# Performance work log

Measured on AMD Instinct MI355X. Metric: run time of the kernel, lower is better.

The kernel has to match this reference:

```python
import jax, jax.numpy as jnp
import numpy as np

L_LAYERS = 2
SEQ = 2048
K_EIG = 24
D = 128
D_TGT = 64
K_U = 3
K_Y = 2
B = 8


def hankel_eigh(n, k):
    # Z[i,j] = 2 / ((i+j)^3 - (i+j)), 1-indexed; top-k eigenpairs
    s = np.arange(1, n + 1, dtype=np.float64)
    ij = s[:, None] + s[None, :]
    z = 2.0 / (ij ** 3 - ij)
    vals, vecs = np.linalg.eigh(z)
    return (jnp.asarray(vals[-k:], jnp.float32), jnp.asarray(vecs[:, -k:], jnp.float32))


def setup_inputs() -> dict:
    key = jax.random.key(0)
    ks = jax.random.split(key, 8)
    sd = 1.0 / np.sqrt(D)
    inp = {
        "x": jax.random.normal(ks[0], (B, SEQ, D), jnp.float32),
        "emb_w": jax.random.normal(ks[1], (D, D), jnp.float32) * sd,
        "emb_b": jnp.zeros((D,), jnp.float32),
        "ln_g": jnp.ones((L_LAYERS, D), jnp.float32),
        "ln_b": jnp.zeros((L_LAYERS, D), jnp.float32),
        "m_phi": jax.random.normal(ks[2], (L_LAYERS, K_EIG * D, D), jnp.float32) * sd,
        "m_u": jax.random.normal(ks[3], (L_LAYERS, D, D, K_U), jnp.float32) * sd,
        "m_y": jax.random.normal(ks[4], (L_LAYERS, D, K_Y, D), jnp.float32) * 0.01,
        "w1": jax.random.normal(ks[5], (L_LAYERS, D, 2 * D), jnp.float32) * sd,
        "b1": jnp.zeros((L_LAYERS, 2 * D), jnp.float32),
        "proj_w": jax.random.normal(ks[6], (D, D_TGT), jnp.float32) * sd,
        "proj_b": jnp.zeros((D_TGT,), jnp.float32),
    }
    ev, evec = hankel_eigh(SEQ, K_EIG)
    inp["eig_vals"] = ev
    inp["eig_vecs"] = evec
    return inp


def compute_x_tilde(x, eig_vals, eig_vecs):
    # x: [B, L, D]; causal (truncated full) convolution of each eigvec filter
    # with each input channel via FFT. Result [B, L, K, D] -> [B, L, K*D].
    n = 2 * SEQ
    V = jnp.fft.rfft(eig_vecs, n=n, axis=0)              # [nf, K]
    U = jnp.fft.rfft(x, n=n, axis=1)                     # [B, nf, D]
    conv = jnp.fft.irfft(V[None, :, :, None] * U[:, :, None, :], n=n, axis=1)[:, :SEQ]
    conv = conv * (eig_vals ** 0.25)[None, None, :, None]
    return conv.reshape(x.shape[0], SEQ, K_EIG * x.shape[-1]).astype(x.dtype)


def compute_ar_x_preds(m_u, x):
    # o[t] = sum_{i<K_U} m_u[:, :, i] @ x[t-i]  (zero for t-i < 0)
    res = jnp.einsum('bli,oi->blo', x, m_u[:, :, 0])
    for i in range(1, K_U):
        xi = jnp.pad(x, ((0, 0), (i, 0), (0, 0)))[:, :SEQ]
        res = res + jnp.einsum('bli,oi->blo', xi, m_u[:, :, i])
    return res


def compute_y_t(m_y, deltas):
    # y[t] = sum_{j<K_Y} m_y[:, j, :] @ y[t-1-j] + deltas[t]
    d = deltas.shape[-1]
    def step(carry, x):  # carry [B, K_Y, d] holds y[t-1], y[t-2], ...
        out = jnp.einsum('okd,bkd->bo', m_y, carry) + x
        carry = jnp.concatenate([out[:, None, :], carry[:, :-1]], axis=1)
        return carry, out
    init = jnp.zeros((deltas.shape[0], K_Y, d), deltas.dtype)
    _, ys = jax.lax.scan(step, init, jnp.swapaxes(deltas, 0, 1))
    return jnp.swapaxes(ys, 0, 1)


def layer_norm(x, g, b):
    mu = x.mean(-1, keepdims=True)
    var = ((x - mu) ** 2).mean(-1, keepdims=True)
    return (x - mu) / jnp.sqrt(var + 1e-5) * g + b


def reference(x, emb_w, emb_b, ln_g, ln_b, m_phi, m_u, m_y, w1, b1, proj_w, proj_b, eig_vals, eig_vecs):
    h = x @ emb_w + emb_b
    for i in range(L_LAYERS):
        z = h
        h = layer_norm(h, ln_g[i], ln_b[i])
        x_tilde = compute_x_tilde(h, eig_vals, eig_vecs)       # [B, L, K*D]
        delta = x_tilde @ m_phi[i] + compute_ar_x_preds(m_u[i], h)
        y = compute_y_t(m_y[i], delta)
        y = jax.nn.gelu(y, approximate=False)
        y = y @ w1[i] + b1[i]
        a, g = jnp.split(y, 2, axis=-1)
        h = a * jax.nn.sigmoid(g) + z                          # GLU + residual (dropout=0)
    return h @ proj_w + proj_b
```

## Files before the change

### kernel.cpp

```cpp
#include <hip/hip_runtime.h>

typedef unsigned short u16;
typedef unsigned int u32;
typedef __bf16 bf16x8 __attribute__((ext_vector_type(8)));
typedef float f32x4 __attribute__((ext_vector_type(4)));
typedef float f32x2 __attribute__((ext_vector_type(2)));
typedef u16 u16x4 __attribute__((ext_vector_type(4)));
typedef u16 u16x8 __attribute__((ext_vector_type(8)));

#define DEV static __device__ __forceinline__

static constexpr int ROWS = 8 * 2048;
static constexpr int TAPS = 24;
static constexpr int PADR = 64;
static constexpr int DROWS = 2048 + PADR;

DEV u16 f2bf(float x) {
  u32 u = __float_as_uint(x);
  u += 0x7fffu + ((u >> 16) & 1u);
  return (u16)(u >> 16);
}

DEV void gld_lds16(const u16* g, u16* l) {
  __builtin_amdgcn_global_load_lds(
      (const __attribute__((address_space(1))) u32*)g,
      (__attribute__((address_space(3))) u32*)l, 16, 0, 0);
}


__global__ void prep_toeplitz(const float* __restrict__ evec,
                              const float* __restrict__ evals,
                              u16* __restrict__ T) {
  int k = blockIdx.x / 33, ti = blockIdx.x % 33;
  float sc = powf(evals[k], 0.25f);
  u16* out = T + (size_t)blockIdx.x * 4096;
  for (int e = threadIdx.x; e < 4096; e += 256) {
    int i = e >> 6, j = e & 63;
    int tau = (ti - 1) * 64 + i - j;
    float v = (tau >= 0 && tau < 2048) ? evec[tau * 24 + k] * sc : 0.f;
    out[e] = f2bf(v);
  }
}

__global__ void transpose_w(const float* __restrict__ src, u16* __restrict__ dst,
                            int K, int N) {
  int idx = blockIdx.x * 256 + threadIdx.x;
  if (idx >= K * N) return;
  int n = idx / K, k = idx % K;
  dst[idx] = f2bf(src[(size_t)k * N + n]);
}

__global__ void prep_mphiT(const float* __restrict__ mphi,
                           const float* __restrict__ mu,
                           u16* __restrict__ dst) {
  int idx = blockIdx.x * 256 + threadIdx.x;
  if (idx >= 128 * 3456) return;
  int o = idx / 3456, c = idx % 3456;
  float v;
  if (c < 3072) {
    v = mphi[(size_t)c * 128 + o];
  } else {
    int cc = c - 3072;
    int j = cc >> 7, i = cc & 127;
    v = mu[((size_t)o * 128 + i) * 3 + j];
  }
  dst[idx] = f2bf(v);
}

__global__ void f32_to_bf16_k(const float* __restrict__ src, u16* __restrict__ dst,
                              int n4) {
  int i = blockIdx.x * 256 + threadIdx.x;
  if (i >= n4) return;
  f32x4 v = *(const f32x4*)(src + (size_t)i * 4);
  u16x4 o;
  o[0] = f2bf(v[0]); o[1] = f2bf(v[1]); o[2] = f2bf(v[2]); o[3] = f2bf(v[3]);
  *(u16x4*)(dst + (size_t)i * 4) = o;
}

__global__ __launch_bounds__(128) void hprep_kernel(const float* __restrict__ my,
                                                    u16* __restrict__ Hp) {
  const int l = blockIdx.x >> 7, j = blockIdx.x & 127;
  const int o = threadIdx.x;
  const float* M = my + (size_t)l * 32768;
  u32 mp1[64], mp2[64];
  {
    const float* r1 = M + (size_t)o * 256;
    const float* r2 = r1 + 128;
#pragma unroll
    for (int q = 0; q < 64; ++q) {
      mp1[q] = (u32)f2bf(r1[2 * q]) | ((u32)f2bf(r1[2 * q + 1]) << 16);
      mp2[q] = (u32)f2bf(r2[2 * q]) | ((u32)f2bf(r2[2 * q + 1]) << 16);
    }
  }
  __shared__ float vb[3][128];
  u16* HpL = Hp + ((size_t)l * 128 + o) * (TAPS * 128) + j;
  float v0 = (o == j) ? 1.f : 0.f;
  vb[0][o] = v0;
  vb[2][o] = 0.f;
  HpL[0] = f2bf(v0);
  __syncthreads();
  for (int tau = 1; tau < TAPS; ++tau) {
    const int a = (tau + 2) % 3;
    const int b = (tau + 1) % 3;
    const int c = tau % 3;
    const float* v1 = vb[a];
    const float* v2 = vb[b];
    float acc = 0.f;
#pragma unroll
    for (int q = 0; q < 64; ++q) {
      u32 w1 = mp1[q], w2 = mp2[q];
      float m1lo = __uint_as_float(w1 << 16);
      float m1hi = __uint_as_float(w1 & 0xffff0000u);
      float m2lo = __uint_as_float(w2 << 16);
      float m2hi = __uint_as_float(w2 & 0xffff0000u);
      acc += m1lo * v1[2 * q] + m1hi * v1[2 * q + 1];
      acc += m2lo * v2[2 * q] + m2hi * v2[2 * q + 1];
    }
    vb[c][o] = acc;
    HpL[tau * 128] = f2bf(acc);
    __syncthreads();
  }
}

__global__ void zero_pad(u16* __restrict__ dpad) {
  int i = blockIdx.x * 256 + threadIdx.x;
  int b = i >> 10, off = i & 1023;
  *(u16x8*)(dpad + (size_t)b * DROWS * 128 + off * 8) = (u16x8){0, 0, 0, 0, 0, 0, 0, 0};
}


__global__ __launch_bounds__(256) void ln_tr_kernel(
    const float* __restrict__ h, const float* __restrict__ gam,
    const float* __restrict__ bet, u16* __restrict__ hlnbf,
    u16* __restrict__ hlnT) {
  __shared__ u16 tile[64][136];
  const int b = blockIdx.x >> 5, st = blockIdx.x & 31;
  const int wrow = threadIdx.x >> 6;
  const int lane = threadIdx.x & 63;
  f32x2 g2 = *(const f32x2*)(gam + lane * 2);
  f32x2 b2 = *(const f32x2*)(bet + lane * 2);
#pragma unroll 4
  for (int it = 0; it < 16; ++it) {
    int lr = it * 4 + wrow;
    size_t row = (size_t)b * 2048 + st * 64 + lr;
    f32x2 v = *(const f32x2*)(h + row * 128 + lane * 2);
    float s = v[0] + v[1];
#pragma unroll
    for (int o = 32; o; o >>= 1) s += __shfl_xor(s, o);
    float mu = s * (1.f / 128.f);
    float dx = v[0] - mu, dy = v[1] - mu;
    float q = dx * dx + dy * dy;
#pragma unroll
    for (int o = 32; o; o >>= 1) q += __shfl_xor(q, o);
    float rstd = rsqrtf(q * (1.f / 128.f) + 1e-5f);
    float o0 = dx * rstd * g2[0] + b2[0];
    float o1 = dy * rstd * g2[1] + b2[1];
    u32 pk = (u32)f2bf(o0) | ((u32)f2bf(o1) << 16);
    *(u32*)(hlnbf + row * 128 + lane * 2) = pk;
    *(u32*)&tile[lr][lane * 2] = pk;
  }
  __syncthreads();
  const int d = threadIdx.x >> 1;
  const int half = threadIdx.x & 1;
#pragma unroll
  for (int i = 0; i < 4; ++i) {
    int sg = half * 4 + i;
    u16x8 w;
#pragma unroll
    for (int j = 0; j < 8; ++j) w[j] = tile[sg * 8 + j][d];
    *(u16x8*)(hlnT + ((size_t)b * 128 + d) * 2048 + st * 64 + sg * 8) = w;
  }
}

__global__ void shift_kernel(const u16* __restrict__ hln, u16* __restrict__ xtc) {
  int row = blockIdx.x;
  int t = row & 2047;
  int d = threadIdx.x;
#pragma unroll
  for (int j = 0; j < 3; ++j) {
    u16 v = (t >= j) ? hln[(size_t)(row - j) * 128 + d] : (u16)0;
    xtc[(size_t)row * 3456 + 3072 + j * 128 + d] = v;
  }
}


template <int BM, int BN, int WROWS, int WCOLS>
__global__ __launch_bounds__(256) void gemm_bt(
    const u16* __restrict__ A, int lda, const u16* __restrict__ BT, int ldbt,
    float* __restrict__ C, int ldc, const float* __restrict__ bias, int kBlocks,
    u16* __restrict__ Cbf) {
  constexpr int WTM = BM / WROWS;
  constexpr int WTN = BN / WCOLS;
  constexpr int FM = WTM / 16;
  constexpr int FN = WTN / 16;
  static_assert(FM >= 1 && FN >= 1, "tile too small");
  __shared__ u16 As[BM * 64];
  __shared__ u16 Bs[BN * 64];
  const int tid = threadIdx.x;
  const int wid = tid >> 6, lane = tid & 63;
  const int bm = blockIdx.x, bn = blockIdx.y;
  const int wr = wid / WCOLS, wc = wid % WCOLS;
  const int r = lane & 15, hi = lane >> 4;

  f32x4 acc[FM][FN];
#pragma unroll
  for (int i = 0; i < FM; ++i)
#pragma unroll
    for (int j = 0; j < FN; ++j) acc[i][j] = (f32x4){0.f, 0.f, 0.f, 0.f};

  for (int kb = 0; kb < kBlocks; ++kb) {
    if (kb) __syncthreads();
#pragma unroll
    for (int it = 0; it < BM / 32; ++it) {
      int ci = it * 256 + tid;
      int sc = (ci & 7) ^ ((ci >> 3) & 7);
      gld_lds16(A + (size_t)(bm * BM + (ci >> 3)) * lda + kb * 64 + sc * 8,
                &As[(it * 256 + wid * 64) * 8]);
    }
#pragma unroll
    for (int it = 0; it < BN / 32; ++it) {
      int ci = it * 256 + tid;
      int sc = (ci & 7) ^ ((ci >> 3) & 7);
      gld_lds16(BT + (size_t)(bn * BN + (ci >> 3)) * ldbt + kb * 64 + sc * 8,
                &Bs[(it * 256 + wid * 64) * 8]);
    }
    __syncthreads();
#pragma unroll
    for (int ks = 0; ks < 2; ++ks) {
      const int sk = ((ks * 4 + hi) ^ (r & 7)) << 3;
      bf16x8 af[FM], bfv[FN];
#pragma unroll
      for (int fm = 0; fm < FM; ++fm)
        af[fm] = *(const bf16x8*)&As[(wr * WTM + fm * 16 + r) * 64 + sk];
#pragma unroll
      for (int fn = 0; fn < FN; ++fn)
        bfv[fn] = *(const bf16x8*)&Bs[(wc * WTN + fn * 16 + r) * 64 + sk];
#pragma unroll
      for (int fm = 0; fm < FM; ++fm)
#pragma unroll
        for (int fn = 0; fn < FN; ++fn)
          acc[fm][fn] = __builtin_amdgcn_mfma_f32_16x16x32_bf16(
              af[fm], bfv[fn], acc[fm][fn], 0, 0, 0);
    }
  }
#pragma unroll
  for (int fm = 0; fm < FM; ++fm) {
#pragma unroll
    for (int fn = 0; fn < FN; ++fn) {
      const int col = bn * BN + wc * WTN + fn * 16 + r;
      const float bv = bias ? bias[col] : 0.f;
#pragma unroll
      for (int q = 0; q < 4; ++q) {
        const int row = bm * BM + wr * WTM + fm * 16 + hi * 4 + q;
        float v = acc[fm][fn][q] + bv;
        if (Cbf) {
          int bb = row >> 11, t = row & 2047;
          Cbf[((size_t)(bb * DROWS + PADR + t)) * 128 + col] = f2bf(v);
        } else {
          C[(size_t)row * ldc + col] = v;
        }
      }
    }
  }
}

__global__ __launch_bounds__(256) void gemm_conv(
    const u16* __restrict__ T, const u16* __restrict__ hlnT,
    u16* __restrict__ xtc) {
  __shared__ u16 As[128 * 64];
  __shared__ u16 Bs[128 * 64];
  const int tid = threadIdx.x;
  const int wid = tid >> 6, lane = tid & 63;
  const int tt = blockIdx.x / 192;
  const int rem = blockIdx.x % 192;
  const int kc = rem >> 3, b = rem & 7;
  const int t0 = (15 - tt) << 7;
  const int r = lane & 15, hi = lane >> 4;
  const int wr = wid >> 1, wc = wid & 1;

  f32x4 acc[4][4];
#pragma unroll
  for (int i = 0; i < 4; ++i)
#pragma unroll
    for (int j = 0; j < 4; ++j) acc[i][j] = (f32x4){0.f, 0.f, 0.f, 0.f};

  const u16* Tk = T + (size_t)kc * 33 * 4096;
  const u16* Bb = hlnT + (size_t)b * 128 * 2048;
  const int nsb = (t0 >> 6) + 2;

  for (int sb = 0; sb < nsb; ++sb) {
    const int dlt = (t0 >> 6) - sb;
    if (sb) __syncthreads();
#pragma unroll
    for (int it = 0; it < 4; ++it) {
      int ci = it * 256 + tid;
      int ti = (ci < 512) ? (dlt + 1) : (dlt + 2);
      int lc = ci & 511;
      int sc = (lc & 7) ^ ((lc >> 3) & 7);
      gld_lds16(Tk + (size_t)ti * 4096 + (lc >> 3) * 64 + sc * 8,
                &As[(it * 256 + wid * 64) * 8]);
    }
#pragma unroll
    for (int it = 0; it < 4; ++it) {
      int ci = it * 256 + tid;
      int sc = (ci & 7) ^ ((ci >> 3) & 7);
      gld_lds16(Bb + (size_t)(ci >> 3) * 2048 + sb * 64 + sc * 8,
                &Bs[(it * 256 + wid * 64) * 8]);
    }
    __syncthreads();
#pragma unroll
    for (int ks = 0; ks < 2; ++ks) {
      const int sk = ((ks * 4 + hi) ^ (r & 7)) << 3;
      bf16x8 af[4], bfv[4];
#pragma unroll
      for (int fm = 0; fm < 4; ++fm)
        af[fm] = *(const bf16x8*)&As[(wr * 64 + fm * 16 + r) * 64 + sk];
#pragma unroll
      for (int fn = 0; fn < 4; ++fn)
        bfv[fn] = *(const bf16x8*)&Bs[(wc * 64 + fn * 16 + r) * 64 + sk];
#pragma unroll
      for (int fm = 0; fm < 4; ++fm)
#pragma unroll
        for (int fn = 0; fn < 4; ++fn)
          acc[fm][fn] = __builtin_amdgcn_mfma_f32_16x16x32_bf16(
              af[fm], bfv[fn], acc[fm][fn], 0, 0, 0);
    }
  }
#pragma unroll
  for (int fm = 0; fm < 4; ++fm) {
#pragma unroll
    for (int fn = 0; fn < 4; ++fn) {
      const int col = wc * 64 + fn * 16 + r;
#pragma unroll
      for (int q = 0; q < 4; ++q) {
        const int row = t0 + wr * 64 + fm * 16 + hi * 4 + q;
        xtc[((size_t)(b * 2048 + row)) * 3456 + kc * 128 + col] = f2bf(acc[fm][fn][q]);
      }
    }
  }
}

__global__ __launch_bounds__(256) void gemm_yconv(
    const u16* __restrict__ dpad, const u16* __restrict__ Hp,
    u16* __restrict__ ybf) {
  __shared__ u16 As[64 * 64];
  __shared__ u16 Bs[64 * 64];
  const int tid = threadIdx.x;
  const int wid = tid >> 6, lane = tid & 63;
  const int bm = blockIdx.x, bn = blockIdx.y;
  const int b = bm >> 5, t0 = (bm & 31) << 6;
  const int r = lane & 15, hi = lane >> 4;

  f32x4 acc[4];
#pragma unroll
  for (int j = 0; j < 4; ++j) acc[j] = (f32x4){0.f, 0.f, 0.f, 0.f};

  const u16* Ab = dpad + (size_t)b * DROWS * 128;
  for (int kb = 0; kb < TAPS * 2; ++kb) {
    const int tap = kb >> 1, i0 = (kb & 1) << 6;
    const u16* Ap = Ab + (size_t)(PADR + t0 - tap) * 128 + i0;
    if (kb) __syncthreads();
#pragma unroll
    for (int it = 0; it < 2; ++it) {
      int ci = it * 256 + tid;
      int sc = (ci & 7) ^ ((ci >> 3) & 7);
      gld_lds16(Ap + (size_t)(ci >> 3) * 128 + sc * 8,
                &As[(it * 256 + wid * 64) * 8]);
    }
#pragma unroll
    for (int it = 0; it < 2; ++it) {
      int ci = it * 256 + tid;
      int sc = (ci & 7) ^ ((ci >> 3) & 7);
      gld_lds16(Hp + (size_t)(bn * 64 + (ci >> 3)) * (TAPS * 128) + kb * 64 + sc * 8,
                &Bs[(it * 256 + wid * 64) * 8]);
    }
    __syncthreads();
#pragma unroll
    for (int ks = 0; ks < 2; ++ks) {
      const int sk = ((ks * 4 + hi) ^ (r & 7)) << 3;
      bf16x8 af = *(const bf16x8*)&As[(wid * 16 + r) * 64 + sk];
      bf16x8 bfv[4];
#pragma unroll
      for (int fn = 0; fn < 4; ++fn)
        bfv[fn] = *(const bf16x8*)&Bs[(fn * 16 + r) * 64 + sk];
#pragma unroll
      for (int fn = 0; fn < 4; ++fn)
        acc[fn] = __builtin_amdgcn_mfma_f32_16x16x32_bf16(af, bfv[fn], acc[fn], 0, 0, 0);
    }
  }
#pragma unroll
  for (int fn = 0; fn < 4; ++fn) {
    const int col = bn * 64 + fn * 16 + r;
#pragma unroll
    for (int q = 0; q < 4; ++q) {
      const int row = t0 + wid * 16 + hi * 4 + q;
      float v = acc[fn][q];
      float gl = 0.5f * v * (1.f + erff(v * 0.70710678118654752f));
      ybf[((size_t)(b * 2048 + row)) * 128 + col] = f2bf(gl);
    }
  }
}

__global__ __launch_bounds__(256) void gemm_w1glu(
    const u16* __restrict__ ybf, const u16* __restrict__ w1T,
    const float* __restrict__ b1, float* __restrict__ h,
    u16* __restrict__ hbf) {
  __shared__ u16 As[32 * 64];
  __shared__ u16 Bs[256 * 64];
  __shared__ float sg[32][128];
  const int tid = threadIdx.x;
  const int wid = tid >> 6, lane = tid & 63;
  const int bm = blockIdx.x;
  const int wr = wid >> 1, wc = wid & 1;
  const int r = lane & 15, hi = lane >> 4;

  f32x4 acc[8];
#pragma unroll
  for (int j = 0; j < 8; ++j) acc[j] = (f32x4){0.f, 0.f, 0.f, 0.f};

  for (int kb = 0; kb < 2; ++kb) {
    if (kb) __syncthreads();
    {
      int ci = tid;
      int sc = (ci & 7) ^ ((ci >> 3) & 7);
      gld_lds16(ybf + (size_t)(bm * 32 + (ci >> 3)) * 128 + kb * 64 + sc * 8,
                &As[(wid * 64) * 8]);
    }
#pragma unroll
    for (int it = 0; it < 8; ++it) {
      int ci = it * 256 + tid;
      int sc = (ci & 7) ^ ((ci >> 3) & 7);
      gld_lds16(w1T + (size_t)(ci >> 3) * 128 + kb * 64 + sc * 8,
                &Bs[(it * 256 + wid * 64) * 8]);
    }
    __syncthreads();
#pragma unroll
    for (int ks = 0; ks < 2; ++ks) {
      const int sk = ((ks * 4 + hi) ^ (r & 7)) << 3;
      bf16x8 af = *(const bf16x8*)&As[(wr * 16 + r) * 64 + sk];
      bf16x8 bfv[8];
#pragma unroll
      for (int fn = 0; fn < 8; ++fn)
        bfv[fn] = *(const bf16x8*)&Bs[(wc * 128 + fn * 16 + r) * 64 + sk];
#pragma unroll
      for (int fn = 0; fn < 8; ++fn)
        acc[fn] = __builtin_amdgcn_mfma_f32_16x16x32_bf16(af, bfv[fn], acc[fn], 0, 0, 0);
    }
  }
  __syncthreads();
  if (wc == 1) {
#pragma unroll
    for (int fn = 0; fn < 8; ++fn) {
      const int colg = fn * 16 + r;
      const float bv = b1[128 + colg];
#pragma unroll
      for (int q = 0; q < 4; ++q) {
        const int rl = wr * 16 + hi * 4 + q;
        float v = acc[fn][q] + bv;
        sg[rl][colg] = 1.f / (1.f + expf(-v));
      }
    }
  }
  __syncthreads();
  if (wc == 0) {
#pragma unroll
    for (int fn = 0; fn < 8; ++fn) {
      const int col = fn * 16 + r;
      const float bv = b1[col];
#pragma unroll
      for (int q = 0; q < 4; ++q) {
        const int rl = wr * 16 + hi * 4 + q;
        const size_t row = (size_t)bm * 32 + rl;
        float a = acc[fn][q] + bv;
        float hn = a * sg[rl][col] + h[row * 128 + col];
        h[row * 128 + col] = hn;
        hbf[row * 128 + col] = f2bf(hn);
      }
    }
  }
}


extern "C" void kernel_launch(void* const* d_in, const int* in_sizes, int n_in,
                              void* d_out, int out_size, void* d_ws, size_t ws_size,
                              hipStream_t stream) {
  (void)in_sizes; (void)n_in; (void)out_size; (void)ws_size;
  const float* x = (const float*)d_in[0];
  const float* emb_w = (const float*)d_in[1];
  const float* emb_b = (const float*)d_in[2];
  const float* ln_g = (const float*)d_in[3];
  const float* ln_b = (const float*)d_in[4];
  const float* m_phi = (const float*)d_in[5];
  const float* m_u = (const float*)d_in[6];
  const float* m_y = (const float*)d_in[7];
  const float* w1 = (const float*)d_in[8];
  const float* b1 = (const float*)d_in[9];
  const float* proj_w = (const float*)d_in[10];
  const float* proj_b = (const float*)d_in[11];
  const float* evals = (const float*)d_in[12];
  const float* evec = (const float*)d_in[13];
  float* out = (float*)d_out;

  char* p = (char*)d_ws;
  auto carve = [&](size_t bytes) {
    char* r = p;
    p += (bytes + 255) & ~(size_t)255;
    return r;
  };
  u16* Tbuf = (u16*)carve((size_t)24 * 33 * 4096 * 2);
  u16* embT = (u16*)carve(128 * 128 * 2);
  u16* w1T = (u16*)carve((size_t)2 * 256 * 128 * 2);
  u16* projT = (u16*)carve(64 * 128 * 2);
  u16* mphiT = (u16*)carve((size_t)2 * 128 * 3456 * 2);
  u16* Hp = (u16*)carve((size_t)2 * 128 * TAPS * 128 * 2);
  u16* xbf = (u16*)carve((size_t)ROWS * 128 * 2);
  float* h = (float*)carve((size_t)ROWS * 128 * 4);
  u16* hbf = (u16*)carve((size_t)ROWS * 128 * 2);
  u16* hlnbf = (u16*)carve((size_t)ROWS * 128 * 2);
  u16* hlnT = (u16*)carve((size_t)ROWS * 128 * 2);
  u16* xtc = (u16*)carve((size_t)ROWS * 3456 * 2);
  u16* dpad = (u16*)carve((size_t)8 * DROWS * 128 * 2);
  u16* ybf = (u16*)carve((size_t)ROWS * 128 * 2);

  prep_toeplitz<<<dim3(24 * 33), dim3(256), 0, stream>>>(evec, evals, Tbuf);
  hprep_kernel<<<dim3(256), dim3(128), 0, stream>>>(m_y, Hp);
  zero_pad<<<dim3(32), dim3(256), 0, stream>>>(dpad);
  transpose_w<<<dim3(64), dim3(256), 0, stream>>>(emb_w, embT, 128, 128);
  transpose_w<<<dim3(128), dim3(256), 0, stream>>>(w1, w1T, 128, 256);
  transpose_w<<<dim3(128), dim3(256), 0, stream>>>(w1 + 128 * 256, w1T + 256 * 128, 128, 256);
  transpose_w<<<dim3(32), dim3(256), 0, stream>>>(proj_w, projT, 128, 64);
  prep_mphiT<<<dim3(1728), dim3(256), 0, stream>>>(m_phi, m_u, mphiT);
  prep_mphiT<<<dim3(1728), dim3(256), 0, stream>>>(
      m_phi + (size_t)3072 * 128, m_u + (size_t)128 * 128 * 3, mphiT + (size_t)128 * 3456);
  f32_to_bf16_k<<<dim3(2048), dim3(256), 0, stream>>>(x, xbf, ROWS * 128 / 4);

  gemm_bt<32, 128, 2, 2><<<dim3(512, 1), dim3(256), 0, stream>>>(
      xbf, 128, embT, 128, h, 128, emb_b, 2, nullptr);

  for (int l = 0; l < 2; ++l) {
    const u16* mT = mphiT + (size_t)l * 128 * 3456;
    ln_tr_kernel<<<dim3(256), dim3(256), 0, stream>>>(
        h, ln_g + l * 128, ln_b + l * 128, hlnbf, hlnT);
    shift_kernel<<<dim3(16384), dim3(128), 0, stream>>>(hlnbf, xtc);
    gemm_conv<<<dim3(3072), dim3(256), 0, stream>>>(Tbuf, hlnT, xtc);
    gemm_bt<32, 128, 2, 2><<<dim3(512, 1), dim3(256), 0, stream>>>(
        xtc, 3456, mT, 3456, nullptr, 0, nullptr, 54, dpad);
    gemm_yconv<<<dim3(256, 2), dim3(256), 0, stream>>>(
        dpad, Hp + (size_t)l * 128 * TAPS * 128, ybf);
    gemm_w1glu<<<dim3(512), dim3(256), 0, stream>>>(
        ybf, w1T + (size_t)l * 256 * 128, b1 + l * 256, h, hbf);
  }

  gemm_bt<32, 64, 2, 2><<<dim3(512, 1), dim3(256), 0, stream>>>(
      hbf, 128, projT, 128, out, 64, proj_b, 2, nullptr);
}
```

Measured before the change: 506.7 us.

## Merge prep kernels, fuse shift into layernorm, double-buffer delta and conv GEMMs

Merges the weight-transpose, conversion and zero-padding prep kernels into one prep_misc launch. The layernorm kernel now writes the shifted autoregressive columns straight into xtc, which removes shift_kernel and the hlnbf buffer. The delta GEMM becomes a dedicated double-buffered kernel that writes bf16 into the padded buffer. gemm_conv reuses the Toeplitz tile from the previous step through a ping-pong A buffer, halving its A loads, and gemm_yconv processes a full 128-wide tap per iteration, halving the sync count. These changes add LDS use and index complexity in exchange for fewer launches and less memory traffic.

```diff
diff --git a/kernel.cpp b/kernel.cpp
--- a/kernel.cpp
+++ b/kernel.cpp
@@ -40,41 +40,6 @@
     float v = (tau >= 0 && tau < 2048) ? evec[tau * 24 + k] * sc : 0.f;
     out[e] = f2bf(v);
   }
-}
-
-__global__ void transpose_w(const float* __restrict__ src, u16* __restrict__ dst,
-                            int K, int N) {
-  int idx = blockIdx.x * 256 + threadIdx.x;
-  if (idx >= K * N) return;
-  int n = idx / K, k = idx % K;
-  dst[idx] = f2bf(src[(size_t)k * N + n]);
-}
-
-__global__ void prep_mphiT(const float* __restrict__ mphi,
-                           const float* __restrict__ mu,
-                           u16* __restrict__ dst) {
-  int idx = blockIdx.x * 256 + threadIdx.x;
-  if (idx >= 128 * 3456) return;
-  int o = idx / 3456, c = idx % 3456;
-  float v;
-  if (c < 3072) {
-    v = mphi[(size_t)c * 128 + o];
-  } else {
-    int cc = c - 3072;
-    int j = cc >> 7, i = cc & 127;
-    v = mu[((size_t)o * 128 + i) * 3 + j];
-  }
-  dst[idx] = f2bf(v);
-}
-
-__global__ void f32_to_bf16_k(const float* __restrict__ src, u16* __restrict__ dst,
-                              int n4) {
-  int i = blockIdx.x * 256 + threadIdx.x;
-  if (i >= n4) return;
-  f32x4 v = *(const f32x4*)(src + (size_t)i * 4);
-  u16x4 o;
-  o[0] = f2bf(v[0]); o[1] = f2bf(v[1]); o[2] = f2bf(v[2]); o[3] = f2bf(v[3]);
-  *(u16x4*)(dst + (size_t)i * 4) = o;
 }
 
 __global__ __launch_bounds__(128) void hprep_kernel(const float* __restrict__ my,
@@ -122,17 +87,67 @@
   }
 }
 
-__global__ void zero_pad(u16* __restrict__ dpad) {
-  int i = blockIdx.x * 256 + threadIdx.x;
-  int b = i >> 10, off = i & 1023;
-  *(u16x8*)(dpad + (size_t)b * DROWS * 128 + off * 8) = (u16x8){0, 0, 0, 0, 0, 0, 0, 0};
+__global__ __launch_bounds__(256) void prep_misc(
+    const float* __restrict__ emb_w, const float* __restrict__ w1,
+    const float* __restrict__ proj_w, const float* __restrict__ mphi,
+    const float* __restrict__ mu, const float* __restrict__ x,
+    u16* __restrict__ embT, u16* __restrict__ w1T, u16* __restrict__ projT,
+    u16* __restrict__ mphiT, u16* __restrict__ xbf, u16* __restrict__ dpad,
+    u16* __restrict__ xtc) {
+  const int blk = blockIdx.x, tid = threadIdx.x;
+  if (blk < 64) {
+    int idx = blk * 256 + tid;
+    int n = idx >> 7, k = idx & 127;
+    embT[idx] = f2bf(emb_w[k * 128 + n]);
+  } else if (blk < 320) {
+    int l = (blk - 64) >> 7;
+    int idx = ((blk - 64) & 127) * 256 + tid;
+    int n = idx >> 7, k = idx & 127;
+    w1T[l * 32768 + idx] = f2bf(w1[l * 32768 + k * 256 + n]);
+  } else if (blk < 352) {
+    int idx = (blk - 320) * 256 + tid;
+    int n = idx >> 7, k = idx & 127;
+    projT[idx] = f2bf(proj_w[k * 64 + n]);
+  } else if (blk < 3808) {
+    int l = (blk - 352) / 1728;
+    int idx = ((blk - 352) % 1728) * 256 + tid;
+    int o = idx / 3456, c = idx % 3456;
+    float v;
+    if (c < 3072) {
+      v = mphi[(size_t)l * 3072 * 128 + (size_t)c * 128 + o];
+    } else {
+      int cc = c - 3072;
+      int j = cc >> 7, i = cc & 127;
+      v = mu[(size_t)l * 128 * 128 * 3 + ((size_t)o * 128 + i) * 3 + j];
+    }
+    mphiT[(size_t)l * 128 * 3456 + idx] = f2bf(v);
+  } else if (blk < 5856) {
+    int i = (blk - 3808) * 256 + tid;
+    f32x4 v = *(const f32x4*)(x + (size_t)i * 4);
+    u16x4 o;
+    o[0] = f2bf(v[0]); o[1] = f2bf(v[1]); o[2] = f2bf(v[2]); o[3] = f2bf(v[3]);
+    *(u16x4*)(xbf + (size_t)i * 4) = o;
+  } else if (blk < 5888) {
+    int i = (blk - 5856) * 256 + tid;
+    int b = i >> 10, off = i & 1023;
+    *(u16x8*)(dpad + (size_t)b * DROWS * 128 + off * 8) =
+        (u16x8){0, 0, 0, 0, 0, 0, 0, 0};
+  } else {
+    for (int e = tid; e < 3072; e += 256) {
+      int b = e / 384, r = e % 384;
+      size_t addr;
+      if (r < 256) addr = ((size_t)b * 2048 + 0) * 3456 + 3200 + r;
+      else addr = ((size_t)b * 2048 + 1) * 3456 + 3328 + (r - 256);
+      xtc[addr] = 0;
+    }
+  }
 }
 
 
 __global__ __launch_bounds__(256) void ln_tr_kernel(
     const float* __restrict__ h, const float* __restrict__ gam,
-    const float* __restrict__ bet, u16* __restrict__ hlnbf,
-    u16* __restrict__ hlnT) {
+    const float* __restrict__ bet, u16* __restrict__ hlnT,
+    u16* __restrict__ xtc) {
   __shared__ u16 tile[64][136];
   const int b = blockIdx.x >> 5, st = blockIdx.x & 31;
   const int wrow = threadIdx.x >> 6;
@@ -142,7 +157,8 @@
 #pragma unroll 4
   for (int it = 0; it < 16; ++it) {
     int lr = it * 4 + wrow;
-    size_t row = (size_t)b * 2048 + st * 64 + lr;
+    int t = st * 64 + lr;
+    size_t row = (size_t)b * 2048 + t;
     f32x2 v = *(const f32x2*)(h + row * 128 + lane * 2);
     float s = v[0] + v[1];
 #pragma unroll
@@ -156,8 +172,10 @@
     float o0 = dx * rstd * g2[0] + b2[0];
     float o1 = dy * rstd * g2[1] + b2[1];
     u32 pk = (u32)f2bf(o0) | ((u32)f2bf(o1) << 16);
-    *(u32*)(hlnbf + row * 128 + lane * 2) = pk;
     *(u32*)&tile[lr][lane * 2] = pk;
+    *(u32*)&xtc[row * 3456 + 3072 + lane * 2] = pk;
+    if (t + 1 < 2048) *(u32*)&xtc[(row + 1) * 3456 + 3200 + lane * 2] = pk;
+    if (t + 2 < 2048) *(u32*)&xtc[(row + 2) * 3456 + 3328 + lane * 2] = pk;
   }
   __syncthreads();
   const int d = threadIdx.x >> 1;
@@ -172,23 +190,11 @@
   }
 }
 
-__global__ void shift_kernel(const u16* __restrict__ hln, u16* __restrict__ xtc) {
-  int row = blockIdx.x;
-  int t = row & 2047;
-  int d = threadIdx.x;
-#pragma unroll
-  for (int j = 0; j < 3; ++j) {
-    u16 v = (t >= j) ? hln[(size_t)(row - j) * 128 + d] : (u16)0;
-    xtc[(size_t)row * 3456 + 3072 + j * 128 + d] = v;
-  }
-}
-
 
 template <int BM, int BN, int WROWS, int WCOLS>
 __global__ __launch_bounds__(256) void gemm_bt(
     const u16* __restrict__ A, int lda, const u16* __restrict__ BT, int ldbt,
-    float* __restrict__ C, int ldc, const float* __restrict__ bias, int kBlocks,
-    u16* __restrict__ Cbf) {
+    float* __restrict__ C, int ldc, const float* __restrict__ bias, int kBlocks) {
   constexpr int WTM = BM / WROWS;
   constexpr int WTN = BN / WCOLS;
   constexpr int FM = WTM / 16;
@@ -252,14 +258,70 @@
 #pragma unroll
       for (int q = 0; q < 4; ++q) {
         const int row = bm * BM + wr * WTM + fm * 16 + hi * 4 + q;
-        float v = acc[fm][fn][q] + bv;
-        if (Cbf) {
-          int bb = row >> 11, t = row & 2047;
-          Cbf[((size_t)(bb * DROWS + PADR + t)) * 128 + col] = f2bf(v);
-        } else {
-          C[(size_t)row * ldc + col] = v;
-        }
+        C[(size_t)row * ldc + col] = acc[fm][fn][q] + bv;
       }
+    }
+  }
+}
+
+__global__ __launch_bounds__(256) void gemm_delta(
+    const u16* __restrict__ A, const u16* __restrict__ BT,
+    u16* __restrict__ dpad) {
+  __shared__ u16 As[2][32 * 64];
+  __shared__ u16 Bs[2][128 * 64];
+  const int tid = threadIdx.x;
+  const int wid = tid >> 6, lane = tid & 63;
+  const int bm = blockIdx.x;
+  const int wr = wid >> 1, wc = wid & 1;
+  const int r = lane & 15, hi = lane >> 4;
+
+  f32x4 acc[4];
+#pragma unroll
+  for (int j = 0; j < 4; ++j) acc[j] = (f32x4){0.f, 0.f, 0.f, 0.f};
+
+  auto stage = [&](int kb, int p) {
+    {
+      int ci = tid;
+      int sc = (ci & 7) ^ ((ci >> 3) & 7);
+      gld_lds16(A + (size_t)(bm * 32 + (ci >> 3)) * 3456 + kb * 64 + sc * 8,
+                &As[p][(wid * 64) * 8]);
+    }
+#pragma unroll
+    for (int it = 0; it < 4; ++it) {
+      int ci = it * 256 + tid;
+      int sc = (ci & 7) ^ ((ci >> 3) & 7);
+      gld_lds16(BT + (size_t)(ci >> 3) * 3456 + kb * 64 + sc * 8,
+                &Bs[p][(it * 256 + wid * 64) * 8]);
+    }
+  };
+
+  stage(0, 0);
+  __syncthreads();
+  for (int kb = 0; kb < 54; ++kb) {
+    const int p = kb & 1;
+    if (kb < 53) stage(kb + 1, p ^ 1);
+#pragma unroll
+    for (int ks = 0; ks < 2; ++ks) {
+      const int sk = ((ks * 4 + hi) ^ (r & 7)) << 3;
+      bf16x8 af = *(const bf16x8*)&As[p][(wr * 16 + r) * 64 + sk];
+      bf16x8 bfv[4];
+#pragma unroll
+      for (int fn = 0; fn < 4; ++fn)
+        bfv[fn] = *(const bf16x8*)&Bs[p][(wc * 64 + fn * 16 + r) * 64 + sk];
+#pragma unroll
+      for (int fn = 0; fn < 4; ++fn)
+        acc[fn] = __builtin_amdgcn_mfma_f32_16x16x32_bf16(af, bfv[fn], acc[fn], 0, 0, 0);
+    }
+    __syncthreads();
+  }
+#pragma unroll
+  for (int fn = 0; fn < 4; ++fn) {
+    const int col = wc * 64 + fn * 16 + r;
+#pragma unroll
+    for (int q = 0; q < 4; ++q) {
+      const int row = bm * 32 + wr * 16 + hi * 4 + q;
+      int bb = row >> 11, t = row & 2047;
+      dpad[((size_t)(bb * DROWS + PADR + t)) * 128 + col] = f2bf(acc[fn][q]);
     }
   }
 }
@@ -267,7 +329,7 @@
 __global__ __launch_bounds__(256) void gemm_conv(
     const u16* __restrict__ T, const u16* __restrict__ hlnT,
     u16* __restrict__ xtc) {
-  __shared__ u16 As[128 * 64];
+  __shared__ u16 As[2][64 * 64];
   __shared__ u16 Bs[128 * 64];
   const int tid = threadIdx.x;
   const int wid = tid >> 6, lane = tid & 63;
@@ -286,19 +348,28 @@
 
   const u16* Tk = T + (size_t)kc * 33 * 4096;
   const u16* Bb = hlnT + (size_t)b * 128 * 2048;
-  const int nsb = (t0 >> 6) + 2;
+  const int base = t0 >> 6;
+  const int nsb = base + 2;
 
   for (int sb = 0; sb < nsb; ++sb) {
-    const int dlt = (t0 >> 6) - sb;
+    const int dlt = base - sb;
+    const int p = sb & 1;
     if (sb) __syncthreads();
 #pragma unroll
-    for (int it = 0; it < 4; ++it) {
-      int ci = it * 256 + tid;
-      int ti = (ci < 512) ? (dlt + 1) : (dlt + 2);
-      int lc = ci & 511;
-      int sc = (lc & 7) ^ ((lc >> 3) & 7);
-      gld_lds16(Tk + (size_t)ti * 4096 + (lc >> 3) * 64 + sc * 8,
-                &As[(it * 256 + wid * 64) * 8]);
+    for (int it = 0; it < 2; ++it) {
+      int ci = it * 256 + tid;
+      int sc = (ci & 7) ^ ((ci >> 3) & 7);
+      gld_lds16(Tk + (size_t)(dlt + 1) * 4096 + (ci >> 3) * 64 + sc * 8,
+                &As[p][(it * 256 + wid * 64) * 8]);
+    }
+    if (sb == 0) {
+#pragma unroll
+      for (int it = 0; it < 2; ++it) {
+        int ci = it * 256 + tid;
+        int sc = (ci & 7) ^ ((ci >> 3) & 7);
+        gld_lds16(Tk + (size_t)(dlt + 2) * 4096 + (ci >> 3) * 64 + sc * 8,
+                  &As[1][(it * 256 + wid * 64) * 8]);
+      }
     }
 #pragma unroll
     for (int it = 0; it < 4; ++it) {
@@ -308,13 +379,14 @@
                 &Bs[(it * 256 + wid * 64) * 8]);
     }
     __syncthreads();
+    const u16* Aw = As[p ^ wr];
 #pragma unroll
     for (int ks = 0; ks < 2; ++ks) {
       const int sk = ((ks * 4 + hi) ^ (r & 7)) << 3;
       bf16x8 af[4], bfv[4];
 #pragma unroll
       for (int fm = 0; fm < 4; ++fm)
-        af[fm] = *(const bf16x8*)&As[(wr * 64 + fm * 16 + r) * 64 + sk];
+        af[fm] = *(const bf16x8*)&Aw[(fm * 16 + r) * 64 + sk];
 #pragma unroll
       for (int fn = 0; fn < 4; ++fn)
         bfv[fn] = *(const bf16x8*)&Bs[(wc * 64 + fn * 16 + r) * 64 + sk];
@@ -343,8 +415,8 @@
 __global__ __launch_bounds__(256) void gemm_yconv(
     const u16* __restrict__ dpad, const u16* __restrict__ Hp,
     u16* __restrict__ ybf) {
-  __shared__ u16 As[64 * 64];
-  __shared__ u16 Bs[64 * 64];
+  __shared__ u16 As[64 * 128];
+  __shared__ u16 Bs[64 * 128];
   const int tid = threadIdx.x;
   const int wid = tid >> 6, lane = tid & 63;
   const int bm = blockIdx.x, bn = blockIdx.y;
@@ -356,33 +428,34 @@
   for (int j = 0; j < 4; ++j) acc[j] = (f32x4){0.f, 0.f, 0.f, 0.f};
 
   const u16* Ab = dpad + (size_t)b * DROWS * 128;
-  for (int kb = 0; kb < TAPS * 2; ++kb) {
-    const int tap = kb >> 1, i0 = (kb & 1) << 6;
-    const u16* Ap = Ab + (size_t)(PADR + t0 - tap) * 128 + i0;
-    if (kb) __syncthreads();
-#pragma unroll
-    for (int it = 0; it < 2; ++it) {
-      int ci = it * 256 + tid;
-      int sc = (ci & 7) ^ ((ci >> 3) & 7);
-      gld_lds16(Ap + (size_t)(ci >> 3) * 128 + sc * 8,
+  for (int tap = 0; tap < TAPS; ++tap) {
+    const u16* Ap = Ab + (size_t)(PADR + t0 - tap) * 128;
+    if (tap) __syncthreads();
+#pragma unroll
+    for (int it = 0; it < 4; ++it) {
+      int ci = it * 256 + tid;
+      int row = ci >> 4;
+      int sc = (ci & 15) ^ (row & 7);
+      gld_lds16(Ap + (size_t)row * 128 + sc * 8,
                 &As[(it * 256 + wid * 64) * 8]);
     }
 #pragma unroll
-    for (int it = 0; it < 2; ++it) {
-      int ci = it * 256 + tid;
-      int sc = (ci & 7) ^ ((ci >> 3) & 7);
-      gld_lds16(Hp + (size_t)(bn * 64 + (ci >> 3)) * (TAPS * 128) + kb * 64 + sc * 8,
+    for (int it = 0; it < 4; ++it) {
+      int ci = it * 256 + tid;
+      int row = ci >> 4;
+      int sc = (ci & 15) ^ (row & 7);
+      gld_lds16(Hp + (size_t)(bn * 64 + row) * (TAPS * 128) + tap * 128 + sc * 8,
                 &Bs[(it * 256 + wid * 64) * 8]);
     }
     __syncthreads();
 #pragma unroll
-    for (int ks = 0; ks < 2; ++ks) {
+    for (int ks = 0; ks < 4; ++ks) {
       const int sk = ((ks * 4 + hi) ^ (r & 7)) << 3;
-      bf16x8 af = *(const bf16x8*)&As[(wid * 16 + r) * 64 + sk];
+      bf16x8 af = *(const bf16x8*)&As[(wid * 16 + r) * 128 + sk];
       bf16x8 bfv[4];
 #pragma unroll
       for (int fn = 0; fn < 4; ++fn)
-        bfv[fn] = *(const bf16x8*)&Bs[(fn * 16 + r) * 64 + sk];
+        bfv[fn] = *(const bf16x8*)&Bs[(fn * 16 + r) * 128 + sk];
 #pragma unroll
       for (int fn = 0; fn < 4; ++fn)
         acc[fn] = __builtin_amdgcn_mfma_f32_16x16x32_bf16(af, bfv[fn], acc[fn], 0, 0, 0);
@@ -516,7 +589,6 @@
   u16* xbf = (u16*)carve((size_t)ROWS * 128 * 2);
   float* h = (float*)carve((size_t)ROWS * 128 * 4);
   u16* hbf = (u16*)carve((size_t)ROWS * 128 * 2);
-  u16* hlnbf = (u16*)carve((size_t)ROWS * 128 * 2);
   u16* hlnT = (u16*)carve((size_t)ROWS * 128 * 2);
   u16* xtc = (u16*)carve((size_t)ROWS * 3456 * 2);
   u16* dpad = (u16*)carve((size_t)8 * DROWS * 128 * 2);
@@ -524,27 +596,18 @@
 
   prep_toeplitz<<<dim3(24 * 33), dim3(256), 0, stream>>>(evec, evals, Tbuf);
   hprep_kernel<<<dim3(256), dim3(128), 0, stream>>>(m_y, Hp);
-  zero_pad<<<dim3(32), dim3(256), 0, stream>>>(dpad);
-  transpose_w<<<dim3(64), dim3(256), 0, stream>>>(emb_w, embT, 128, 128);
-  transpose_w<<<dim3(128), dim3(256), 0, stream>>>(w1, w1T, 128, 256);
-  transpose_w<<<dim3(128), dim3(256), 0, stream>>>(w1 + 128 * 256, w1T + 256 * 128, 128, 256);
-  transpose_w<<<dim3(32), dim3(256), 0, stream>>>(proj_w, projT, 128, 64);
-  prep_mphiT<<<dim3(1728), dim3(256), 0, stream>>>(m_phi, m_u, mphiT);
-  prep_mphiT<<<dim3(1728), dim3(256), 0, stream>>>(
-      m_phi + (size_t)3072 * 128, m_u + (size_t)128 * 128 * 3, mphiT + (size_t)128 * 3456);
-  f32_to_bf16_k<<<dim3(2048), dim3(256), 0, stream>>>(x, xbf, ROWS * 128 / 4);
+  prep_misc<<<dim3(5889), dim3(256), 0, stream>>>(
+      emb_w, w1, proj_w, m_phi, m_u, x, embT, w1T, projT, mphiT, xbf, dpad, xtc);
 
   gemm_bt<32, 128, 2, 2><<<dim3(512, 1), dim3(256), 0, stream>>>(
-      xbf, 128, embT, 128, h, 128, emb_b, 2, nullptr);
+      xbf, 128, embT, 128, h, 128, emb_b, 2);
 
   for (int l = 0; l < 2; ++l) {
     const u16* mT = mphiT + (size_t)l * 128 * 3456;
     ln_tr_kernel<<<dim3(256), dim3(256), 0, stream>>>(
-        h, ln_g + l * 128, ln_b + l * 128, hlnbf, hlnT);
-    shift_kernel<<<dim3(16384), dim3(128), 0, stream>>>(hlnbf, xtc);
+        h, ln_g + l * 128, ln_b + l * 128, hlnT, xtc);
     gemm_conv<<<dim3(3072), dim3(256), 0, stream>>>(Tbuf, hlnT, xtc);
-    gemm_bt<32, 128, 2, 2><<<dim3(512, 1), dim3(256), 0, stream>>>(
-        xtc, 3456, mT, 3456, nullptr, 0, nullptr, 54, dpad);
+    gemm_delta<<<dim3(512), dim3(256), 0, stream>>>(xtc, mT, dpad);
     gemm_yconv<<<dim3(256, 2), dim3(256), 0, stream>>>(
         dpad, Hp + (size_t)l * 128 * TAPS * 128, ybf);
     gemm_w1glu<<<dim3(512), dim3(256), 0, stream>>>(
@@ -552,5 +615,5 @@
   }
 
   gemm_bt<32, 64, 2, 2><<<dim3(512, 1), dim3(256), 0, stream>>>(
-      hbf, 128, projT, 128, out, 64, proj_b, 2, nullptr);
-}
+      hbf, 128, projT, 128, out, 64, proj_b, 2);
+}
```

New measurement: 465.6 us. 1.09x faster.
